# Performance work log

Measured on AMD Instinct MI355X. Metric: run time of the kernel, lower is better.

## Reference

```python
import jax, jax.numpy as jnp
import numpy as np

D_MODEL = 512
D_STATE = 16
D_CONV = 4
EXPAND = 2
D_INNER = EXPAND * D_MODEL          # 1024
DT_RANK = (D_MODEL + 15) // 16      # 32
B, L = 32, 2048
EPS = 1e-12


def _ln(x, g, b):
    mu = jnp.mean(x, axis=-1, keepdims=True)
    var = jnp.mean(jnp.square(x - mu), axis=-1, keepdims=True)
    return (x - mu) * jax.lax.rsqrt(var + EPS) * g + b


def setup_inputs() -> dict:
    key = jax.random.key(0)
    ks = jax.random.split(key, 12)
    s = lambda fan: 1.0 / np.sqrt(fan)
    inp = {
        "input_tensor": jax.random.normal(ks[0], (B, L, D_MODEL), jnp.float32),
        # Mamba params
        "in_proj_w": jax.random.normal(ks[1], (2 * D_INNER, D_MODEL), jnp.float32) * s(D_MODEL),
        "conv_w": jax.random.normal(ks[2], (D_INNER, D_CONV), jnp.float32) * s(D_CONV),
        "conv_b": jnp.zeros((D_INNER,), jnp.float32),
        "x_proj_w": jax.random.normal(ks[3], (DT_RANK + 2 * D_STATE, D_INNER), jnp.float32) * s(D_INNER),
        "dt_proj_w": jax.random.normal(ks[4], (D_INNER, DT_RANK), jnp.float32) * s(DT_RANK),
        "dt_proj_b": jnp.full((D_INNER,), -4.0, jnp.float32),  # softplus(-4) ~ small dt
        "A_log": jnp.log(jnp.broadcast_to(jnp.arange(1, D_STATE + 1, dtype=jnp.float32), (D_INNER, D_STATE))),
        "D": jnp.ones((D_INNER,), jnp.float32),
        "out_proj_w": jax.random.normal(ks[5], (D_MODEL, D_INNER), jnp.float32) * s(D_INNER),
        # block params
        "ln1_g": jnp.ones((D_MODEL,), jnp.float32),
        "ln1_b": jnp.zeros((D_MODEL,), jnp.float32),
        "w1_w": jax.random.normal(ks[6], (4 * D_MODEL, D_MODEL), jnp.float32) * s(D_MODEL),
        "w1_b": jnp.zeros((4 * D_MODEL,), jnp.float32),
        "w2_w": jax.random.normal(ks[7], (D_MODEL, 4 * D_MODEL), jnp.float32) * s(4 * D_MODEL),
        "w2_b": jnp.zeros((D_MODEL,), jnp.float32),
        "ln2_g": jnp.ones((D_MODEL,), jnp.float32),
        "ln2_b": jnp.zeros((D_MODEL,), jnp.float32),
    }
    return inp


def _mamba(x, in_proj_w, conv_w, conv_b, x_proj_w, dt_proj_w, dt_proj_b, A_log, D, out_proj_w):
    # x: [B, L, d_model]
    xz = jnp.einsum("bld,ed->ble", x, in_proj_w)          # [B,L,2*d_inner]
    xi, z = jnp.split(xz, 2, axis=-1)                      # each [B,L,d_inner]

    # depthwise causal conv1d along L (d_conv taps)
    xpad = jnp.pad(xi, ((0, 0), (D_CONV - 1, 0), (0, 0)))
    conv = conv_b
    for k in range(D_CONV):
        conv = conv + xpad[:, k:k + L, :] * conv_w[:, k]
    u = jax.nn.silu(conv)                                  # [B,L,d_inner]

    # input-dependent dt, B, C
    x_dbl = jnp.einsum("bld,ed->ble", u, x_proj_w)         # [B,L,dt_rank+2N]
    dt, B_t, C_t = jnp.split(x_dbl, [DT_RANK, DT_RANK + D_STATE], axis=-1)
    delta = jax.nn.softplus(jnp.einsum("blr,dr->bld", dt, dt_proj_w) + dt_proj_b)  # [B,L,d_inner]

    A = -jnp.exp(A_log)                                    # [d_inner, N]

    def step(h, inp):
        u_t, d_t, Bt, Ct = inp                             # [B,d_in],[B,d_in],[B,N],[B,N]
        dA = jnp.exp(d_t[..., None] * A)                   # [B,d_in,N]
        h = h * dA + (d_t * u_t)[..., None] * Bt[:, None, :]
        y = jnp.sum(h * Ct[:, None, :], axis=-1)           # [B,d_in]
        return h, y

    h0 = jnp.zeros((B, D_INNER, D_STATE), u.dtype)
    xs = (jnp.swapaxes(u, 0, 1), jnp.swapaxes(delta, 0, 1),
          jnp.swapaxes(B_t, 0, 1), jnp.swapaxes(C_t, 0, 1))
    _, ys = jax.lax.scan(step, h0, xs)                     # [L,B,d_inner]
    y = jnp.swapaxes(ys, 0, 1) + u * D
    y = y * jax.nn.silu(z)
    return jnp.einsum("ble,de->bld", y, out_proj_w)        # [B,L,d_model]


def reference(input_tensor, in_proj_w, conv_w, conv_b, x_proj_w, dt_proj_w, dt_proj_b,
              A_log, D, out_proj_w, ln1_g, ln1_b, w1_w, w1_b, w2_w, w2_b, ln2_g, ln2_b):
    h = _mamba(input_tensor, in_proj_w, conv_w, conv_b, x_proj_w, dt_proj_w,
               dt_proj_b, A_log, D, out_proj_w)
    h = _ln(h + input_tensor, ln1_g, ln1_b)                # num_layers > 1 branch, dropout=0
    f = jax.nn.gelu(jnp.einsum("bld,fd->blf", h, w1_w) + w1_b, approximate=False)
    f = jnp.einsum("blf,df->bld", f, w2_w) + w2_b
    return _ln(f + h, ln2_g, ln2_b)
```

## Files before the change

kernel.cpp:

```cpp
#include <hip/hip_runtime.h>
#include <hip/hip_bf16.h>

#define DM 512
#define DI 1024
#define DC 4
#define DTR 32
#define NST 16
#define LSEQ 2048
#define NBATCH 32
#define NCH 16
#define CHL 128

typedef __attribute__((ext_vector_type(8))) short b16x8;
typedef __attribute__((ext_vector_type(4))) float fx4;
typedef __attribute__((ext_vector_type(4))) unsigned short u16x4;

__device__ __forceinline__ unsigned short f2bf(float f) {
    union { float f; unsigned u; } x; x.f = f;
    unsigned r = x.u + 0x7fffu + ((x.u >> 16) & 1u);
    return (unsigned short)(r >> 16);
}
__device__ __forceinline__ float bf2f(unsigned short u) {
    union { unsigned u; float f; } x; x.u = ((unsigned)u) << 16;
    return x.f;
}

__global__ __launch_bounds__(256) void cast_kernel(const float* __restrict__ src,
                                                   unsigned short* __restrict__ dst, int n4) {
    int i = blockIdx.x * 256 + threadIdx.x;
    if (i < n4) {
        fx4 v = *(const fx4*)&src[(size_t)i * 4];
        u16x4 o;
        #pragma unroll
        for (int j = 0; j < 4; j++) o[j] = f2bf(v[j]);
        *(u16x4*)&dst[(size_t)i * 4] = o;
    }
}

__global__ __launch_bounds__(256) void extract_dt_kernel(const float* __restrict__ xdbl,
                                                         unsigned short* __restrict__ dt16) {
    int i = blockIdx.x * 256 + threadIdx.x;
    int m = i >> 5, r = i & 31;
    dt16[i] = f2bf(xdbl[(size_t)m * 64 + r]);
}

template <int BN, int BK, int EPI, bool HAS_BIAS>
__global__ __launch_bounds__(256, 2) void gemm_bf16(const unsigned short* __restrict__ A,
                                                    const unsigned short* __restrict__ W,
                                                    const float* __restrict__ bias,
                                                    void* __restrict__ Cout, int N, int K) {
    constexpr int BM = 128;
    constexpr int GPR = BK / 8;
    __shared__ __align__(16) unsigned short As[BM * BK];
    __shared__ __align__(16) unsigned short Ws[BN * BK];
    const int tid = threadIdx.x;
    const int wave = tid >> 6, lane = tid & 63;
    const int lr = lane & 15, lg = lane >> 4;
    const int ntx = gridDim.x;
    const int tot = ntx * gridDim.y;
    const int lin = blockIdx.y * ntx + blockIdx.x;
    const int cpx = tot >> 3;
    const int swz = (lin & 7) * cpx + (lin >> 3);
    const int m0 = (swz / ntx) * BM, n0 = (swz % ntx) * BN;
    const int wm0 = (wave >> 1) * 64, wn0 = (wave & 1) * (BN / 2);
    constexpr int NR = BN / 32;
    fx4 acc[4][NR];
    #pragma unroll
    for (int i = 0; i < 4; i++)
        #pragma unroll
        for (int j = 0; j < NR; j++) acc[i][j] = fx4{0.f, 0.f, 0.f, 0.f};

    for (int k0 = 0; k0 < K; k0 += BK) {
        #pragma unroll
        for (int i = 0; i < (BM * BK / 8) / 256; i++) {
            int cb = (i * 4 + wave) * 64, c = cb + lane;
            int row = c / GPR, kk = (c % GPR) * 8;
            const unsigned short* g = A + (size_t)(m0 + row) * K + k0 + kk;
            __builtin_amdgcn_global_load_lds(
                (const __attribute__((address_space(1))) unsigned int*)g,
                (__attribute__((address_space(3))) unsigned int*)&As[cb * 8], 16, 0, 0);
        }
        #pragma unroll
        for (int i = 0; i < (BN * BK / 8) / 256; i++) {
            int cb = (i * 4 + wave) * 64, c = cb + lane;
            int row = c / GPR, kk = (c % GPR) * 8;
            const unsigned short* g = W + (size_t)(n0 + row) * K + k0 + kk;
            __builtin_amdgcn_global_load_lds(
                (const __attribute__((address_space(1))) unsigned int*)g,
                (__attribute__((address_space(3))) unsigned int*)&Ws[cb * 8], 16, 0, 0);
        }
        __syncthreads();
        #pragma unroll
        for (int ks = 0; ks < BK / 32; ks++) {
            b16x8 af[4], bfr[NR];
            #pragma unroll
            for (int mi = 0; mi < 4; mi++)
                af[mi] = *(const b16x8*)&As[(wm0 + mi * 16 + lr) * BK + ks * 32 + lg * 8];
            #pragma unroll
            for (int ni = 0; ni < NR; ni++)
                bfr[ni] = *(const b16x8*)&Ws[(wn0 + ni * 16 + lr) * BK + ks * 32 + lg * 8];
            #pragma unroll
            for (int mi = 0; mi < 4; mi++)
                #pragma unroll
                for (int ni = 0; ni < NR; ni++)
                    acc[mi][ni] = __builtin_amdgcn_mfma_f32_16x16x32_bf16(af[mi], bfr[ni],
                                                                         acc[mi][ni], 0, 0, 0);
        }
        __syncthreads();
    }
    #pragma unroll
    for (int mi = 0; mi < 4; mi++) {
        #pragma unroll
        for (int ni = 0; ni < NR; ni++) {
            #pragma unroll
            for (int j2 = 0; j2 < 4; j2++) {
                int row = m0 + wm0 + mi * 16 + lg * 4 + j2;
                int col = n0 + wn0 + ni * 16 + lr;
                float v = acc[mi][ni][j2];
                if (HAS_BIAS) v += bias[col];
                size_t o = (size_t)row * N + col;
                if (EPI == 0) {
                    ((float*)Cout)[o] = v;
                } else if (EPI == 1) {
                    ((unsigned short*)Cout)[o] = f2bf(v);
                } else if (EPI == 2) {
                    v = 0.5f * v * (1.f + erff(v * 0.70710678118654752f));
                    ((unsigned short*)Cout)[o] = f2bf(v);
                } else if (EPI == 3) {
                    v = (v > 20.f) ? v : log1pf(__expf(v));
                    ((float*)Cout)[o] = v;
                } else {
                    v = (v > 20.f) ? v : log1pf(__expf(v));
                    ((unsigned short*)Cout)[o] = f2bf(v);
                }
            }
        }
    }
}

__global__ __launch_bounds__(256) void conv_silu_kernel(const unsigned short* __restrict__ xz16,
                                                        const float* __restrict__ cw,
                                                        const float* __restrict__ cb,
                                                        unsigned short* __restrict__ u16) {
    int idx = blockIdx.x * 256 + threadIdx.x;
    int m = idx >> 7;
    int d0 = (idx & 127) << 3;
    int l = m & (LSEQ - 1);
    float acc[8];
    fx4 w0[8];
    #pragma unroll
    for (int j = 0; j < 8; j++) {
        acc[j] = cb[d0 + j];
        w0[j] = *(const fx4*)&cw[(d0 + j) * 4];
    }
    #pragma unroll
    for (int k = 0; k < 4; k++) {
        int lm = l - 3 + k;
        if (lm >= 0) {
            b16x8 xv = *(const b16x8*)&xz16[(size_t)(m - 3 + k) * (2 * DI) + d0];
            #pragma unroll
            for (int j = 0; j < 8; j++) acc[j] += bf2f((unsigned short)xv[j]) * w0[j][k];
        }
    }
    b16x8 o;
    #pragma unroll
    for (int j = 0; j < 8; j++) {
        float v = acc[j];
        v = v / (1.f + __expf(-v));
        o[j] = (short)f2bf(v);
    }
    *(b16x8*)&u16[(size_t)m * DI + d0] = o;
}

__device__ __forceinline__ bool load_A(const float* __restrict__ A_log, int d, float* Av) {
    bool fast = true;
    #pragma unroll
    for (int n = 0; n < NST; n++) {
        Av[n] = -__expf(A_log[(size_t)d * NST + n]);
        fast = fast && (fabsf(Av[n] + (float)(n + 1)) < 1e-4f * (float)(n + 1));
    }
    return fast;
}

__device__ __forceinline__ void en_tree(float e1, float* en) {
    float e2 = e1 * e1, e3 = e2 * e1, e4 = e2 * e2, e8 = e4 * e4, e12 = e8 * e4;
    en[0] = e1;        en[1] = e2;        en[2] = e3;        en[3] = e4;
    en[4] = e4 * e1;   en[5] = e4 * e2;   en[6] = e4 * e3;   en[7] = e8;
    en[8] = e8 * e1;   en[9] = e8 * e2;   en[10] = e8 * e3;  en[11] = e12;
    en[12] = e12 * e1; en[13] = e12 * e2; en[14] = e12 * e3; en[15] = e8 * e8;
}

__global__ __launch_bounds__(256) void scan_partial(const unsigned short* __restrict__ delta16,
                                                    const unsigned short* __restrict__ u16,
                                                    const float* __restrict__ xdbl,
                                                    const float* __restrict__ A_log,
                                                    float* __restrict__ sumd,
                                                    float* __restrict__ hend) {
    int d = blockIdx.x * 256 + threadIdx.x;
    int ch = blockIdx.y, b = blockIdx.z;
    size_t bL = (size_t)b * LSEQ + (size_t)ch * CHL;
    float Av[NST], h[NST];
    const bool fast = load_A(A_log, d, Av);
    #pragma unroll
    for (int n = 0; n < NST; n++) h[n] = 0.f;
    float S = 0.f;
    #pragma unroll 2
    for (int l = 0; l < CHL; l++) {
        size_t r = bL + l;
        float dl = bf2f(delta16[r * DI + d]);
        float uu = bf2f(u16[r * DI + d]);
        S += dl;
        float du = dl * uu;
        const float* xr = &xdbl[r * 64 + 32];
        float Bv[NST];
        #pragma unroll
        for (int t = 0; t < 4; t++) *(fx4*)&Bv[t * 4] = *(const fx4*)(xr + t * 4);
        float en[NST];
        if (fast) {
            en_tree(__expf(-dl), en);
        } else {
            #pragma unroll
            for (int n = 0; n < NST; n++) en[n] = __expf(dl * Av[n]);
        }
        #pragma unroll
        for (int n = 0; n < NST; n++) h[n] = h[n] * en[n] + du * Bv[n];
    }
    size_t base = ((size_t)(b * NCH + ch) * NST) * DI + d;
    #pragma unroll
    for (int n = 0; n < NST; n++) hend[base + (size_t)n * DI] = h[n];
    sumd[(size_t)(b * NCH + ch) * DI + d] = S;
}

__global__ __launch_bounds__(256) void scan_carry(const float* __restrict__ sumd,
                                                  const float* __restrict__ hend,
                                                  const float* __restrict__ A_log,
                                                  float* __restrict__ hin) {
    int d = blockIdx.x * 256 + threadIdx.x;
    int b = blockIdx.y;
    float Av[NST], h[NST];
    #pragma unroll
    for (int n = 0; n < NST; n++) {
        Av[n] = -__expf(A_log[(size_t)d * NST + n]);
        h[n] = 0.f;
    }
    for (int k = 0; k < NCH; k++) {
        size_t base = ((size_t)(b * NCH + k) * NST) * DI + d;
        float S = sumd[(size_t)(b * NCH + k) * DI + d];
        #pragma unroll
        for (int n = 0; n < NST; n++) {
            hin[base + (size_t)n * DI] = h[n];
            h[n] = h[n] * __expf(S * Av[n]) + hend[base + (size_t)n * DI];
        }
    }
}

__global__ __launch_bounds__(256) void scan_final(const unsigned short* __restrict__ delta16,
                                                  const unsigned short* u16,
                                                  const unsigned short* __restrict__ xz16,
                                                  const float* __restrict__ xdbl,
                                                  const float* __restrict__ A_log,
                                                  const float* __restrict__ Dp,
                                                  const float* __restrict__ hin,
                                                  unsigned short* y16) {
    int d = blockIdx.x * 256 + threadIdx.x;
    int ch = blockIdx.y, b = blockIdx.z;
    size_t bL = (size_t)b * LSEQ + (size_t)ch * CHL;
    float Av[NST], h[NST];
    const bool fast = load_A(A_log, d, Av);
    size_t base = ((size_t)(b * NCH + ch) * NST) * DI + d;
    #pragma unroll
    for (int n = 0; n < NST; n++) h[n] = hin[base + (size_t)n * DI];
    float Dd = Dp[d];
    #pragma unroll 2
    for (int l = 0; l < CHL; l++) {
        size_t r = bL + l;
        float dl = bf2f(delta16[r * DI + d]);
        float uu = bf2f(u16[r * DI + d]);
        float zz = bf2f(xz16[r * (2 * DI) + DI + d]);
        float du = dl * uu;
        const float* xr = &xdbl[r * 64 + 32];
        float Bv[NST], Cv[NST];
        #pragma unroll
        for (int t = 0; t < 4; t++) {
            *(fx4*)&Bv[t * 4] = *(const fx4*)(xr + t * 4);
            *(fx4*)&Cv[t * 4] = *(const fx4*)(xr + 16 + t * 4);
        }
        float en[NST];
        if (fast) {
            en_tree(__expf(-dl), en);
        } else {
            #pragma unroll
            for (int n = 0; n < NST; n++) en[n] = __expf(dl * Av[n]);
        }
        float y = 0.f;
        #pragma unroll
        for (int n = 0; n < NST; n++) {
            h[n] = h[n] * en[n] + du * Bv[n];
            y += h[n] * Cv[n];
        }
        y = (y + uu * Dd) * (zz / (1.f + __expf(-zz)));
        y16[r * DI + d] = f2bf(y);
    }
}

__global__ __launch_bounds__(256) void ln_kernel(const float* __restrict__ a,
                                                 const float* __restrict__ res,
                                                 const float* __restrict__ g,
                                                 const float* __restrict__ bta,
                                                 float* __restrict__ out32,
                                                 unsigned short* __restrict__ out16) {
    int row = blockIdx.x, tid = threadIdx.x;
    size_t base = (size_t)row * DM;
    float v0 = a[base + tid] + res[base + tid];
    float v1 = a[base + tid + 256] + res[base + tid + 256];
    float s = v0 + v1, q = v0 * v0 + v1 * v1;
    #pragma unroll
    for (int m = 32; m >= 1; m >>= 1) {
        s += __shfl_xor(s, m);
        q += __shfl_xor(q, m);
    }
    __shared__ float rs[4], rq[4];
    int wv = tid >> 6;
    if ((tid & 63) == 0) { rs[wv] = s; rq[wv] = q; }
    __syncthreads();
    s = rs[0] + rs[1] + rs[2] + rs[3];
    q = rq[0] + rq[1] + rq[2] + rq[3];
    float mu = s * (1.f / DM);
    float var = q * (1.f / DM) - mu * mu;
    float rsg = rsqrtf(var + 1e-12f);
    float o0 = (v0 - mu) * rsg * g[tid] + bta[tid];
    float o1 = (v1 - mu) * rsg * g[tid + 256] + bta[tid + 256];
    out32[base + tid] = o0;
    out32[base + tid + 256] = o1;
    if (out16) {
        out16[base + tid] = f2bf(o0);
        out16[base + tid + 256] = f2bf(o1);
    }
}

static size_t align256(size_t b) { return (b + 255) & ~(size_t)255; }

static size_t tier_need(size_t Gb) {
    size_t R = Gb * LSEQ;
    size_t w = 0;
    w += align256((size_t)2 * DI * DM * 2);
    w += align256((size_t)64 * DI * 2);
    w += align256((size_t)DM * DI * 2);
    w += align256((size_t)4 * DM * DM * 2);
    w += align256((size_t)DM * 4 * DM * 2);
    w += align256((size_t)DI * DTR * 2);
    w += align256(R * 2048 * 2);
    w += align256(R * 1024 * 2);
    w += align256(R * 1024 * 4);
    w += align256(R * 64 * 4);
    w += align256(R * 32 * 2);
    w += align256(R * 512 * 2);
    w += align256(Gb * NCH * DI * 4);
    w += align256(Gb * NCH * NST * DI * 4);
    w += align256(Gb * NCH * NST * DI * 4);
    return w;
}

extern "C" void kernel_launch(void* const* d_in, const int* in_sizes, int n_in,
                              void* d_out, int out_size, void* d_ws, size_t ws_size,
                              hipStream_t stream) {
    const float* x_in   = (const float*)d_in[0];
    const float* inpw   = (const float*)d_in[1];
    const float* convw  = (const float*)d_in[2];
    const float* convb  = (const float*)d_in[3];
    const float* xprojw = (const float*)d_in[4];
    const float* dtw    = (const float*)d_in[5];
    const float* dtb    = (const float*)d_in[6];
    const float* A_log  = (const float*)d_in[7];
    const float* Dp     = (const float*)d_in[8];
    const float* outpw  = (const float*)d_in[9];
    const float* ln1g   = (const float*)d_in[10];
    const float* ln1b   = (const float*)d_in[11];
    const float* w1w    = (const float*)d_in[12];
    const float* w1b    = (const float*)d_in[13];
    const float* w2w    = (const float*)d_in[14];
    const float* w2b    = (const float*)d_in[15];
    const float* ln2g   = (const float*)d_in[16];
    const float* ln2b   = (const float*)d_in[17];

    int G = 1;
    const int tiers[5] = {32, 16, 8, 4, 2};
    for (int t = 0; t < 5; t++) {
        if (ws_size >= tier_need((size_t)tiers[t])) { G = tiers[t]; break; }
    }
    const size_t R = (size_t)G * LSEQ;

    char* w = (char*)d_ws;
    auto alloc = [&](size_t bytes) { char* p = w; w += align256(bytes); return p; };

    unsigned short* win16 = (unsigned short*)alloc((size_t)2 * DI * DM * 2);
    unsigned short* wxp16 = (unsigned short*)alloc((size_t)64 * DI * 2);
    unsigned short* wop16 = (unsigned short*)alloc((size_t)DM * DI * 2);
    unsigned short* ww116 = (unsigned short*)alloc((size_t)4 * DM * DM * 2);
    unsigned short* ww216 = (unsigned short*)alloc((size_t)DM * 4 * DM * 2);
    unsigned short* wdt16 = (unsigned short*)alloc((size_t)DI * DTR * 2);
    unsigned short* xz16  = (unsigned short*)alloc(R * 2048 * 2);
    unsigned short* u16   = (unsigned short*)alloc(R * 1024 * 2);
    float*          dreg  = (float*)alloc(R * 1024 * 4);
    float*          xdbl  = (float*)alloc(R * 64 * 4);
    unsigned short* dt16  = (unsigned short*)alloc(R * 32 * 2);
    unsigned short* x16   = (unsigned short*)alloc(R * 512 * 2);
    float*          sumd  = (float*)alloc((size_t)G * NCH * DI * 4);
    float*          hend  = (float*)alloc((size_t)G * NCH * NST * DI * 4);
    float*          hin   = (float*)alloc((size_t)G * NCH * NST * DI * 4);

    unsigned short* delta16 = (unsigned short*)dreg;
    unsigned short* y16 = u16;
    unsigned short* f16 = xz16;
    float*          mm32 = dreg;
    float*          h32  = dreg + R * 512;
    float*          w2o  = dreg;
    unsigned short* h16  = x16;

    dim3 blk(256);
    cast_kernel<<<(2 * DI * DM / 4 + 255) / 256, blk, 0, stream>>>(inpw, win16, 2 * DI * DM / 4);
    cast_kernel<<<(64 * DI / 4 + 255) / 256, blk, 0, stream>>>(xprojw, wxp16, 64 * DI / 4);
    cast_kernel<<<(DM * DI / 4 + 255) / 256, blk, 0, stream>>>(outpw, wop16, DM * DI / 4);
    cast_kernel<<<(4 * DM * DM / 4 + 255) / 256, blk, 0, stream>>>(w1w, ww116, 4 * DM * DM / 4);
    cast_kernel<<<(DM * 4 * DM / 4 + 255) / 256, blk, 0, stream>>>(w2w, ww216, DM * 4 * DM / 4);
    cast_kernel<<<(DI * DTR / 4 + 255) / 256, blk, 0, stream>>>(dtw, wdt16, DI * DTR / 4);

    for (int grp = 0; grp < NBATCH / G; grp++) {
        const size_t rb = (size_t)grp * R;
        const float* xg = x_in + rb * DM;
        cast_kernel<<<(int)(R * DM / 4 / 256), blk, 0, stream>>>(xg, x16, (int)(R * DM / 4));
        gemm_bf16<128, 64, 1, false><<<dim3(2 * DI / 128, R / 128), blk, 0, stream>>>(
            x16, win16, nullptr, xz16, 2 * DI, DM);
        conv_silu_kernel<<<(int)(R * (DI / 8) / 256), blk, 0, stream>>>(xz16, convw, convb, u16);
        gemm_bf16<64, 64, 0, false><<<dim3(1, R / 128), blk, 0, stream>>>(
            u16, wxp16, nullptr, xdbl, 64, DI);
        extract_dt_kernel<<<(int)(R * DTR / 256), blk, 0, stream>>>(xdbl, dt16);
        gemm_bf16<128, 32, 4, true><<<dim3(DI / 128, R / 128), blk, 0, stream>>>(
            dt16, wdt16, dtb, delta16, DI, DTR);
        scan_partial<<<dim3(DI / 256, NCH, G), blk, 0, stream>>>(
            delta16, u16, xdbl, A_log, sumd, hend);
        scan_carry<<<dim3(DI / 256, G), blk, 0, stream>>>(sumd, hend, A_log, hin);
        scan_final<<<dim3(DI / 256, NCH, G), blk, 0, stream>>>(
            delta16, u16, xz16, xdbl, A_log, Dp, hin, y16);
        gemm_bf16<128, 64, 0, false><<<dim3(DM / 128, R / 128), blk, 0, stream>>>(
            y16, wop16, nullptr, mm32, DM, DI);
        ln_kernel<<<(int)R, blk, 0, stream>>>(mm32, xg, ln1g, ln1b, h32, h16);
        gemm_bf16<128, 64, 2, true><<<dim3(4 * DM / 128, R / 128), blk, 0, stream>>>(
            h16, ww116, w1b, f16, 4 * DM, DM);
        gemm_bf16<128, 64, 0, true><<<dim3(DM / 128, R / 128), blk, 0, stream>>>(
            f16, ww216, w2b, w2o, DM, 4 * DM);
        ln_kernel<<<(int)R, blk, 0, stream>>>(w2o, h32, ln2g, ln2b,
                                              (float*)d_out + rb * DM, nullptr);
    }
}
```

Baseline: 1.818 ms.

## Store GEMM outputs and LN intermediates in bf16, fold dt extraction into x_proj

The out_proj and w2 GEMMs now write bf16 instead of fp32. The first layernorm emits only a bf16 result, and the second layernorm reads its residual from that bf16 copy instead of an fp32 h32 buffer. The x_proj GEMM gains an epilogue that also writes the bf16 dt slice, which removes the separate extract kernel. The aim is to cut global memory traffic and one launch, at the cost of extra bf16 rounding on the residual path and the pre-LN sums.

```diff
diff --git a/kernel.cpp b/kernel.cpp
--- a/kernel.cpp
+++ b/kernel.cpp
@@ -37,18 +37,12 @@
     }
 }
 
-__global__ __launch_bounds__(256) void extract_dt_kernel(const float* __restrict__ xdbl,
-                                                         unsigned short* __restrict__ dt16) {
-    int i = blockIdx.x * 256 + threadIdx.x;
-    int m = i >> 5, r = i & 31;
-    dt16[i] = f2bf(xdbl[(size_t)m * 64 + r]);
-}
-
 template <int BN, int BK, int EPI, bool HAS_BIAS>
 __global__ __launch_bounds__(256, 2) void gemm_bf16(const unsigned short* __restrict__ A,
                                                     const unsigned short* __restrict__ W,
                                                     const float* __restrict__ bias,
-                                                    void* __restrict__ Cout, int N, int K) {
+                                                    void* __restrict__ Cout, int N, int K,
+                                                    unsigned short* __restrict__ aux) {
     constexpr int BM = 128;
     constexpr int GPR = BK / 8;
     __shared__ __align__(16) unsigned short As[BM * BK];
@@ -129,9 +123,12 @@
                 } else if (EPI == 3) {
                     v = (v > 20.f) ? v : log1pf(__expf(v));
                     ((float*)Cout)[o] = v;
-                } else {
+                } else if (EPI == 4) {
                     v = (v > 20.f) ? v : log1pf(__expf(v));
                     ((unsigned short*)Cout)[o] = f2bf(v);
+                } else {
+                    ((float*)Cout)[o] = v;
+                    if (col < DTR) aux[(size_t)row * DTR + col] = f2bf(v);
                 }
             }
         }
@@ -303,16 +300,30 @@
     }
 }
 
-__global__ __launch_bounds__(256) void ln_kernel(const float* __restrict__ a,
-                                                 const float* __restrict__ res,
+template <int AIN, int RIN, int OUT>
+__global__ __launch_bounds__(256) void ln_kernel(const void* __restrict__ a,
+                                                 const void* __restrict__ res,
                                                  const float* __restrict__ g,
                                                  const float* __restrict__ bta,
-                                                 float* __restrict__ out32,
-                                                 unsigned short* __restrict__ out16) {
+                                                 void* __restrict__ out) {
     int row = blockIdx.x, tid = threadIdx.x;
     size_t base = (size_t)row * DM;
-    float v0 = a[base + tid] + res[base + tid];
-    float v1 = a[base + tid + 256] + res[base + tid + 256];
+    float a0, a1, r0, r1;
+    if (AIN == 0) {
+        a0 = ((const float*)a)[base + tid];
+        a1 = ((const float*)a)[base + tid + 256];
+    } else {
+        a0 = bf2f(((const unsigned short*)a)[base + tid]);
+        a1 = bf2f(((const unsigned short*)a)[base + tid + 256]);
+    }
+    if (RIN == 0) {
+        r0 = ((const float*)res)[base + tid];
+        r1 = ((const float*)res)[base + tid + 256];
+    } else {
+        r0 = bf2f(((const unsigned short*)res)[base + tid]);
+        r1 = bf2f(((const unsigned short*)res)[base + tid + 256]);
+    }
+    float v0 = a0 + r0, v1 = a1 + r1;
     float s = v0 + v1, q = v0 * v0 + v1 * v1;
     #pragma unroll
     for (int m = 32; m >= 1; m >>= 1) {
@@ -330,11 +341,12 @@
     float rsg = rsqrtf(var + 1e-12f);
     float o0 = (v0 - mu) * rsg * g[tid] + bta[tid];
     float o1 = (v1 - mu) * rsg * g[tid + 256] + bta[tid + 256];
-    out32[base + tid] = o0;
-    out32[base + tid + 256] = o1;
-    if (out16) {
-        out16[base + tid] = f2bf(o0);
-        out16[base + tid + 256] = f2bf(o1);
+    if (OUT == 0) {
+        ((float*)out)[base + tid] = o0;
+        ((float*)out)[base + tid + 256] = o1;
+    } else {
+        ((unsigned short*)out)[base + tid] = f2bf(o0);
+        ((unsigned short*)out)[base + tid + 256] = f2bf(o1);
     }
 }
 
@@ -351,7 +363,7 @@
     w += align256((size_t)DI * DTR * 2);
     w += align256(R * 2048 * 2);
     w += align256(R * 1024 * 2);
-    w += align256(R * 1024 * 4);
+    w += align256(R * 1024 * 2);
     w += align256(R * 64 * 4);
     w += align256(R * 32 * 2);
     w += align256(R * 512 * 2);
@@ -401,7 +413,7 @@
     unsigned short* wdt16 = (unsigned short*)alloc((size_t)DI * DTR * 2);
     unsigned short* xz16  = (unsigned short*)alloc(R * 2048 * 2);
     unsigned short* u16   = (unsigned short*)alloc(R * 1024 * 2);
-    float*          dreg  = (float*)alloc(R * 1024 * 4);
+    unsigned short* dreg  = (unsigned short*)alloc(R * 1024 * 2);
     float*          xdbl  = (float*)alloc(R * 64 * 4);
     unsigned short* dt16  = (unsigned short*)alloc(R * 32 * 2);
     unsigned short* x16   = (unsigned short*)alloc(R * 512 * 2);
@@ -409,12 +421,11 @@
     float*          hend  = (float*)alloc((size_t)G * NCH * NST * DI * 4);
     float*          hin   = (float*)alloc((size_t)G * NCH * NST * DI * 4);
 
-    unsigned short* delta16 = (unsigned short*)dreg;
+    unsigned short* delta16 = dreg;
     unsigned short* y16 = u16;
     unsigned short* f16 = xz16;
-    float*          mm32 = dreg;
-    float*          h32  = dreg + R * 512;
-    float*          w2o  = dreg;
+    unsigned short* mm16 = dreg;
+    unsigned short* w2o16 = dreg;
     unsigned short* h16  = x16;
 
     dim3 blk(256);
@@ -430,26 +441,25 @@
         const float* xg = x_in + rb * DM;
         cast_kernel<<<(int)(R * DM / 4 / 256), blk, 0, stream>>>(xg, x16, (int)(R * DM / 4));
         gemm_bf16<128, 64, 1, false><<<dim3(2 * DI / 128, R / 128), blk, 0, stream>>>(
-            x16, win16, nullptr, xz16, 2 * DI, DM);
+            x16, win16, nullptr, xz16, 2 * DI, DM, nullptr);
         conv_silu_kernel<<<(int)(R * (DI / 8) / 256), blk, 0, stream>>>(xz16, convw, convb, u16);
-        gemm_bf16<64, 64, 0, false><<<dim3(1, R / 128), blk, 0, stream>>>(
-            u16, wxp16, nullptr, xdbl, 64, DI);
-        extract_dt_kernel<<<(int)(R * DTR / 256), blk, 0, stream>>>(xdbl, dt16);
+        gemm_bf16<64, 64, 5, false><<<dim3(1, R / 128), blk, 0, stream>>>(
+            u16, wxp16, nullptr, xdbl, 64, DI, dt16);
         gemm_bf16<128, 32, 4, true><<<dim3(DI / 128, R / 128), blk, 0, stream>>>(
-            dt16, wdt16, dtb, delta16, DI, DTR);
+            dt16, wdt16, dtb, delta16, DI, DTR, nullptr);
         scan_partial<<<dim3(DI / 256, NCH, G), blk, 0, stream>>>(
             delta16, u16, xdbl, A_log, sumd, hend);
         scan_carry<<<dim3(DI / 256, G), blk, 0, stream>>>(sumd, hend, A_log, hin);
         scan_final<<<dim3(DI / 256, NCH, G), blk, 0, stream>>>(
             delta16, u16, xz16, xdbl, A_log, Dp, hin, y16);
-        gemm_bf16<128, 64, 0, false><<<dim3(DM / 128, R / 128), blk, 0, stream>>>(
-            y16, wop16, nullptr, mm32, DM, DI);
-        ln_kernel<<<(int)R, blk, 0, stream>>>(mm32, xg, ln1g, ln1b, h32, h16);
+        gemm_bf16<128, 64, 1, false><<<dim3(DM / 128, R / 128), blk, 0, stream>>>(
+            y16, wop16, nullptr, mm16, DM, DI, nullptr);
+        ln_kernel<1, 0, 1><<<(int)R, blk, 0, stream>>>(mm16, xg, ln1g, ln1b, h16);
         gemm_bf16<128, 64, 2, true><<<dim3(4 * DM / 128, R / 128), blk, 0, stream>>>(
-            h16, ww116, w1b, f16, 4 * DM, DM);
-        gemm_bf16<128, 64, 0, true><<<dim3(DM / 128, R / 128), blk, 0, stream>>>(
-            f16, ww216, w2b, w2o, DM, 4 * DM);
-        ln_kernel<<<(int)R, blk, 0, stream>>>(w2o, h32, ln2g, ln2b,
-                                              (float*)d_out + rb * DM, nullptr);
-    }
-}
+            h16, ww116, w1b, f16, 4 * DM, DM, nullptr);
+        gemm_bf16<128, 64, 1, true><<<dim3(DM / 128, R / 128), blk, 0, stream>>>(
+            f16, ww216, w2b, w2o16, DM, 4 * DM, nullptr);
+        ln_kernel<1, 1, 0><<<(int)R, blk, 0, stream>>>(w2o16, h16, ln2g, ln2b,
+                                                       (float*)d_out + rb * DM);
+    }
+}
```

Measured after the change: 1.734 ms. -4.6%, faster.
